# Performance work log

Hardware: AMD Instinct MI355X
Metric: run time of the kernel (lower is better)

## Reference

```python
import jax, jax.numpy as jnp
from jax import lax
import numpy as np

K_IN, K_OUT, K_STATE = 64, 64, 256
T_PRE, T_FWD, BATCH = 64, 80, 4096


def setup_inputs() -> dict:
    key = jax.random.key(0)
    ks = jax.random.split(key, 13)
    s = 0.05  # param scale for numerical stability of the recurrences
    return {
        "pre_x": jax.random.normal(ks[0], (T_PRE, BATCH, K_IN), jnp.float32),
        "pre_y": jax.random.normal(ks[1], (T_PRE, BATCH, K_OUT), jnp.float32),
        "forward_x": jax.random.normal(ks[2], (T_FWD, BATCH, K_IN), jnp.float32),
        "A_w": jax.random.normal(ks[3], (K_STATE, K_STATE), jnp.float32) * s,
        "A_b": jax.random.normal(ks[4], (K_STATE,), jnp.float32) * s,
        "B_w": jax.random.normal(ks[5], (K_STATE, K_IN), jnp.float32) * s,
        "B_b": jax.random.normal(ks[6], (K_STATE,), jnp.float32) * s,
        "C_w": jax.random.normal(ks[7], (K_OUT, K_STATE), jnp.float32) * s,
        "C_b": jax.random.normal(ks[8], (K_OUT,), jnp.float32) * s,
        "W_ih": jax.random.normal(ks[9], (K_STATE, K_IN + K_OUT), jnp.float32) * s,
        "b_ih": jax.random.normal(ks[10], (K_STATE,), jnp.float32) * s,
        "W_hh": jax.random.normal(ks[11], (K_STATE, K_STATE), jnp.float32) * s,
        "b_hh": jax.random.normal(ks[12], (K_STATE,), jnp.float32) * s,
    }


def reference(pre_x, pre_y, forward_x, A_w, A_b, B_w, B_b, C_w, C_b,
              W_ih, b_ih, W_hh, b_hh):
    # --- encoder: single-layer tanh RNN over concat(pre_x, pre_y), h0 = 0 ---
    xy = jnp.concatenate([pre_x, pre_y], axis=2)          # [T_pre, B, k_in+k_out]
    # precompute input projection for all steps (one big GEMM)
    inp_proj = xy @ W_ih.T + b_ih                          # [T_pre, B, k_state]

    def rnn_step(h, u):
        h = jnp.tanh(u + h @ W_hh.T + b_hh)
        return h, None

    h0 = jnp.zeros((pre_x.shape[1], W_hh.shape[0]), pre_x.dtype)
    hn, _ = lax.scan(rnn_step, h0, inp_proj)               # hn: [B, k_state]

    # --- state-space rollout: h_t = A h_{t-1} + B x_t ; y_t = C h_t ---
    Bx = forward_x @ B_w.T + (A_b + B_b)                   # fold both biases once

    def ss_step(h, bx):
        h = h @ A_w.T + bx
        return h, h

    _, hs = lax.scan(ss_step, hn, Bx)                      # [T_fwd, B, k_state]
    return hs @ C_w.T + C_b                                # [T_fwd, B, k_out]
```

## Files before the change

kernel.cpp:

```cpp
#include <hip/hip_runtime.h>

typedef __attribute__((ext_vector_type(8))) short short8;
typedef __attribute__((ext_vector_type(4))) float f32x4;

#define T_PRE 64
#define T_FWD 80
#define BATCHN 4096
#define PITCH 392

#define U_WRNN 0
#define U_WSS  98304
#define U_C    180224
#define U_END  196608
#define PREP_N 197120

__device__ __forceinline__ unsigned short bf1(float a) {
  unsigned ua = __float_as_uint(a);
  return (unsigned short)((ua + 0x7fffu + ((ua >> 16) & 1u)) >> 16);
}
__device__ __forceinline__ unsigned bfpack(float a, float b) {
  unsigned ua = __float_as_uint(a), ub = __float_as_uint(b);
  ua = (ua + 0x7fffu + ((ua >> 16) & 1u)) >> 16;
  ub = (ub + 0x7fffu + ((ub >> 16) & 1u)) >> 16;
  return ua | (ub << 16);
}
__device__ __forceinline__ float tanh_fast(float x) {
  float e = __expf(2.0f * x);
  return 1.0f - 2.0f * __builtin_amdgcn_rcpf(e + 1.0f);
}

__global__ void prep_kernel(const float* __restrict__ A_w, const float* __restrict__ A_b,
                            const float* __restrict__ B_w, const float* __restrict__ B_b,
                            const float* __restrict__ C_w,
                            const float* __restrict__ W_ih, const float* __restrict__ b_ih,
                            const float* __restrict__ W_hh, const float* __restrict__ b_hh,
                            unsigned short* __restrict__ ws) {
  int i = blockIdx.x * 256 + threadIdx.x;
  if (i < U_WSS) {
    int j = i / 384, k = i - j * 384;
    float v = (k < 256) ? W_hh[j * 256 + k] : W_ih[j * 128 + (k - 256)];
    ws[i] = bf1(v);
  } else if (i < U_C) {
    int ii = i - U_WSS;
    int j = ii / 320, k = ii - j * 320;
    float v = (k < 256) ? A_w[j * 256 + k] : B_w[j * 64 + (k - 256)];
    ws[i] = bf1(v);
  } else if (i < U_END) {
    int ii = i - U_C;
    int o = ii >> 8, k = ii & 255;
    ws[i] = bf1(C_w[o * 256 + k]);
  } else if (i < PREP_N) {
    float* fb = (float*)(ws + U_END);
    int j = i - U_END;
    fb[j] = (j < 256) ? (b_ih[j] + b_hh[j]) : (A_b[j - 256] + B_b[j - 256]);
  }
}

__global__ __launch_bounds__(256, 1) void rnn_ss_kernel(
    const float* __restrict__ pre_x, const float* __restrict__ pre_y,
    const float* __restrict__ fwd_x, const float* __restrict__ C_b,
    const unsigned short* __restrict__ ws, float* __restrict__ out) {
  __shared__ unsigned short xh[16 * PITCH];

  const int tid = threadIdx.x;
  const int lane = tid & 63;
  const int w = tid >> 6;
  const int col = lane & 15;
  const int q = lane >> 4;
  const int r0 = blockIdx.x * 16;
  const int srow = tid >> 4;
  const int sc4 = tid & 15;

  {
    unsigned* p = (unsigned*)xh;
#pragma unroll
    for (int it = 0; it < 8; ++it) {
      int i = tid + it * 256;
      int r = i >> 7, c = i & 127;
      p[r * (PITCH / 2) + c] = 0u;
    }
  }

  const float* fbias = (const float*)(ws + U_END);

  {
    short8 wf[4][12];
#pragma unroll
    for (int mt = 0; mt < 4; ++mt)
#pragma unroll
      for (int kf = 0; kf < 12; ++kf)
        wf[mt][kf] = *(const short8*)(ws + U_WRNN +
                       (size_t)(w * 64 + mt * 16 + col) * 384 + kf * 32 + q * 8);
    f32x4 br[4];
#pragma unroll
    for (int mt = 0; mt < 4; ++mt)
      br[mt] = *(const f32x4*)(fbias + w * 64 + mt * 16 + q * 4);

    {
      f32x4 px = *(const f32x4*)(pre_x + (size_t)(r0 + srow) * 64 + sc4 * 4);
      f32x4 py = *(const f32x4*)(pre_y + (size_t)(r0 + srow) * 64 + sc4 * 4);
      *(uint2*)&xh[srow * PITCH + 256 + sc4 * 4] = make_uint2(bfpack(px[0], px[1]), bfpack(px[2], px[3]));
      *(uint2*)&xh[srow * PITCH + 320 + sc4 * 4] = make_uint2(bfpack(py[0], py[1]), bfpack(py[2], py[3]));
    }

    for (int t = 0; t < T_PRE; ++t) {
      f32x4 npx, npy;
      if (t < T_PRE - 1) {
        npx = *(const f32x4*)(pre_x + ((size_t)(t + 1) * BATCHN + r0 + srow) * 64 + sc4 * 4);
        npy = *(const f32x4*)(pre_y + ((size_t)(t + 1) * BATCHN + r0 + srow) * 64 + sc4 * 4);
      }
      __syncthreads();
      short8 bfr[12];
#pragma unroll
      for (int kf = 0; kf < 12; ++kf)
        bfr[kf] = *(const short8*)&xh[col * PITCH + kf * 32 + q * 8];
      f32x4 acc[4];
#pragma unroll
      for (int mt = 0; mt < 4; ++mt) acc[mt] = br[mt];
#pragma unroll
      for (int kf = 0; kf < 12; ++kf)
#pragma unroll
        for (int mt = 0; mt < 4; ++mt)
          acc[mt] = __builtin_amdgcn_mfma_f32_16x16x32_bf16(wf[mt][kf], bfr[kf], acc[mt], 0, 0, 0);
      __syncthreads();
#pragma unroll
      for (int mt = 0; mt < 4; ++mt) {
        float t0 = tanh_fast(acc[mt][0]), t1 = tanh_fast(acc[mt][1]);
        float t2 = tanh_fast(acc[mt][2]), t3 = tanh_fast(acc[mt][3]);
        *(uint2*)&xh[col * PITCH + w * 64 + mt * 16 + q * 4] =
            make_uint2(bfpack(t0, t1), bfpack(t2, t3));
      }
      if (t < T_PRE - 1) {
        *(uint2*)&xh[srow * PITCH + 256 + sc4 * 4] = make_uint2(bfpack(npx[0], npx[1]), bfpack(npx[2], npx[3]));
        *(uint2*)&xh[srow * PITCH + 320 + sc4 * 4] = make_uint2(bfpack(npy[0], npy[1]), bfpack(npy[2], npy[3]));
      }
    }
  }

  {
    short8 sf[4][10];
#pragma unroll
    for (int mt = 0; mt < 4; ++mt)
#pragma unroll
      for (int kf = 0; kf < 10; ++kf)
        sf[mt][kf] = *(const short8*)(ws + U_WSS +
                       (size_t)(w * 64 + mt * 16 + col) * 320 + kf * 32 + q * 8);
    short8 cf[8];
#pragma unroll
    for (int kf = 0; kf < 8; ++kf)
      cf[kf] = *(const short8*)(ws + U_C + (size_t)(w * 16 + col) * 256 + kf * 32 + q * 8);
    f32x4 bs[4];
#pragma unroll
    for (int mt = 0; mt < 4; ++mt)
      bs[mt] = *(const f32x4*)(fbias + 256 + w * 64 + mt * 16 + q * 4);
    f32x4 cb = *(const f32x4*)(C_b + w * 16 + q * 4);

    {
      f32x4 fx = *(const f32x4*)(fwd_x + (size_t)(r0 + srow) * 64 + sc4 * 4);
      *(uint2*)&xh[srow * PITCH + 256 + sc4 * 4] = make_uint2(bfpack(fx[0], fx[1]), bfpack(fx[2], fx[3]));
    }

    for (int i = 0; i < T_FWD; ++i) {
      f32x4 nfx;
      if (i < T_FWD - 1)
        nfx = *(const f32x4*)(fwd_x + ((size_t)(i + 1) * BATCHN + r0 + srow) * 64 + sc4 * 4);
      __syncthreads();
      short8 bfr[10];
#pragma unroll
      for (int kf = 0; kf < 10; ++kf)
        bfr[kf] = *(const short8*)&xh[col * PITCH + kf * 32 + q * 8];
      f32x4 acc[4];
#pragma unroll
      for (int mt = 0; mt < 4; ++mt) acc[mt] = bs[mt];
#pragma unroll
      for (int kf = 0; kf < 10; ++kf)
#pragma unroll
        for (int mt = 0; mt < 4; ++mt)
          acc[mt] = __builtin_amdgcn_mfma_f32_16x16x32_bf16(sf[mt][kf], bfr[kf], acc[mt], 0, 0, 0);
      if (i >= 1) {
        f32x4 y = cb;
#pragma unroll
        for (int kf = 0; kf < 8; ++kf)
          y = __builtin_amdgcn_mfma_f32_16x16x32_bf16(cf[kf], bfr[kf], y, 0, 0, 0);
        *(f32x4*)(out + ((size_t)(i - 1) * BATCHN + r0 + col) * 64 + w * 16 + q * 4) = y;
      }
      __syncthreads();
#pragma unroll
      for (int mt = 0; mt < 4; ++mt)
        *(uint2*)&xh[col * PITCH + w * 64 + mt * 16 + q * 4] =
            make_uint2(bfpack(acc[mt][0], acc[mt][1]), bfpack(acc[mt][2], acc[mt][3]));
      if (i < T_FWD - 1)
        *(uint2*)&xh[srow * PITCH + 256 + sc4 * 4] = make_uint2(bfpack(nfx[0], nfx[1]), bfpack(nfx[2], nfx[3]));
    }

    __syncthreads();
    {
      short8 bfr[8];
#pragma unroll
      for (int kf = 0; kf < 8; ++kf)
        bfr[kf] = *(const short8*)&xh[col * PITCH + kf * 32 + q * 8];
      f32x4 y = cb;
#pragma unroll
      for (int kf = 0; kf < 8; ++kf)
        y = __builtin_amdgcn_mfma_f32_16x16x32_bf16(cf[kf], bfr[kf], y, 0, 0, 0);
      *(f32x4*)(out + ((size_t)(T_FWD - 1) * BATCHN + r0 + col) * 64 + w * 16 + q * 4) = y;
    }
  }
}

extern "C" void kernel_launch(void* const* d_in, const int* in_sizes, int n_in,
                              void* d_out, int out_size, void* d_ws, size_t ws_size,
                              hipStream_t stream) {
  const float* pre_x = (const float*)d_in[0];
  const float* pre_y = (const float*)d_in[1];
  const float* fwd_x = (const float*)d_in[2];
  const float* A_w   = (const float*)d_in[3];
  const float* A_b   = (const float*)d_in[4];
  const float* B_w   = (const float*)d_in[5];
  const float* B_b   = (const float*)d_in[6];
  const float* C_w   = (const float*)d_in[7];
  const float* C_b   = (const float*)d_in[8];
  const float* W_ih  = (const float*)d_in[9];
  const float* b_ih  = (const float*)d_in[10];
  const float* W_hh  = (const float*)d_in[11];
  const float* b_hh  = (const float*)d_in[12];
  unsigned short* ws = (unsigned short*)d_ws;
  float* out = (float*)d_out;

  prep_kernel<<<(PREP_N + 255) / 256, 256, 0, stream>>>(
      A_w, A_b, B_w, B_b, C_w, W_ih, b_ih, W_hh, b_hh, ws);
  rnn_ss_kernel<<<BATCHN / 16, 256, 0, stream>>>(pre_x, pre_y, fwd_x, C_b, ws, out);
}
```

Baseline: 316.4 us.

## Double-buffer recurrent state in LDS and split work across eight waves

Moves the block from 4 to 8 waves, so each wave owns 32 state rows (2 MFMA tiles) rather than 64. The hidden and input buffers are now ping-pong double-buffered, which removes one of the two barriers per timestep. X/Y staging is split across the two thread halves, and bf16 packing now uses the HIP intrinsic. The aim is a shorter serial critical path per step and better latency hiding. In exchange, the C-projection runs on only half the waves, and each step still pays a block-wide barrier across more waves.

```diff
diff --git a/kernel.cpp b/kernel.cpp
--- a/kernel.cpp
+++ b/kernel.cpp
@@ -1,4 +1,5 @@
 #include <hip/hip_runtime.h>
+#include <hip/hip_bf16.h>
 
 typedef __attribute__((ext_vector_type(8))) short short8;
 typedef __attribute__((ext_vector_type(4))) float f32x4;
@@ -6,7 +7,9 @@
 #define T_PRE 64
 #define T_FWD 80
 #define BATCHN 4096
-#define PITCH 392
+
+#define HP 264
+#define IP 136
 
 #define U_WRNN 0
 #define U_WSS  98304
@@ -18,11 +21,11 @@
   unsigned ua = __float_as_uint(a);
   return (unsigned short)((ua + 0x7fffu + ((ua >> 16) & 1u)) >> 16);
 }
-__device__ __forceinline__ unsigned bfpack(float a, float b) {
-  unsigned ua = __float_as_uint(a), ub = __float_as_uint(b);
-  ua = (ua + 0x7fffu + ((ua >> 16) & 1u)) >> 16;
-  ub = (ub + 0x7fffu + ((ub >> 16) & 1u)) >> 16;
-  return ua | (ub << 16);
+__device__ __forceinline__ unsigned pk(float a, float b) {
+  __hip_bfloat162 h = __float22bfloat162_rn(make_float2(a, b));
+  unsigned u;
+  __builtin_memcpy(&u, &h, 4);
+  return u;
 }
 __device__ __forceinline__ float tanh_fast(float x) {
   float e = __expf(2.0f * x);
@@ -56,11 +59,12 @@
   }
 }
 
-__global__ __launch_bounds__(256, 1) void rnn_ss_kernel(
+__global__ __launch_bounds__(512, 1) void rnn_ss_kernel(
     const float* __restrict__ pre_x, const float* __restrict__ pre_y,
     const float* __restrict__ fwd_x, const float* __restrict__ C_b,
     const unsigned short* __restrict__ ws, float* __restrict__ out) {
-  __shared__ unsigned short xh[16 * PITCH];
+  __shared__ unsigned short hbuf[2][16 * HP];
+  __shared__ unsigned short ibuf[2][16 * IP];
 
   const int tid = threadIdx.x;
   const int lane = tid & 63;
@@ -68,137 +72,152 @@
   const int col = lane & 15;
   const int q = lane >> 4;
   const int r0 = blockIdx.x * 16;
-  const int srow = tid >> 4;
+  const int srow = (tid & 255) >> 4;
   const int sc4 = tid & 15;
+  const bool xhalf = (tid >= 256);
+
+#pragma unroll
+  for (int it = 0; it < 2; ++it) {
+    int i = tid + it * 512;
+    int r = i >> 6, c = (i & 63) * 4;
+    *(uint2*)&hbuf[0][r * HP + c] = make_uint2(0u, 0u);
+  }
+
+  const float* fbias = (const float*)(ws + U_END);
+  int cur = 0;
 
   {
-    unsigned* p = (unsigned*)xh;
-#pragma unroll
-    for (int it = 0; it < 8; ++it) {
-      int i = tid + it * 256;
-      int r = i >> 7, c = i & 127;
-      p[r * (PITCH / 2) + c] = 0u;
-    }
-  }
-
-  const float* fbias = (const float*)(ws + U_END);
-
-  {
-    short8 wf[4][12];
-#pragma unroll
-    for (int mt = 0; mt < 4; ++mt)
+    short8 wf[2][12];
+#pragma unroll
+    for (int mt = 0; mt < 2; ++mt)
 #pragma unroll
       for (int kf = 0; kf < 12; ++kf)
         wf[mt][kf] = *(const short8*)(ws + U_WRNN +
-                       (size_t)(w * 64 + mt * 16 + col) * 384 + kf * 32 + q * 8);
-    f32x4 br[4];
-#pragma unroll
-    for (int mt = 0; mt < 4; ++mt)
-      br[mt] = *(const f32x4*)(fbias + w * 64 + mt * 16 + q * 4);
+                       (size_t)(w * 32 + mt * 16 + col) * 384 + kf * 32 + q * 8);
+    f32x4 br[2];
+#pragma unroll
+    for (int mt = 0; mt < 2; ++mt)
+      br[mt] = *(const f32x4*)(fbias + w * 32 + mt * 16 + q * 4);
 
     {
-      f32x4 px = *(const f32x4*)(pre_x + (size_t)(r0 + srow) * 64 + sc4 * 4);
-      f32x4 py = *(const f32x4*)(pre_y + (size_t)(r0 + srow) * 64 + sc4 * 4);
-      *(uint2*)&xh[srow * PITCH + 256 + sc4 * 4] = make_uint2(bfpack(px[0], px[1]), bfpack(px[2], px[3]));
-      *(uint2*)&xh[srow * PITCH + 320 + sc4 * 4] = make_uint2(bfpack(py[0], py[1]), bfpack(py[2], py[3]));
+      f32x4 v = xhalf ? *(const f32x4*)(pre_x + (size_t)(r0 + srow) * 64 + sc4 * 4)
+                      : *(const f32x4*)(pre_y + (size_t)(r0 + srow) * 64 + sc4 * 4);
+      *(uint2*)&ibuf[0][srow * IP + (xhalf ? 0 : 64) + sc4 * 4] =
+          make_uint2(pk(v[0], v[1]), pk(v[2], v[3]));
     }
 
     for (int t = 0; t < T_PRE; ++t) {
-      f32x4 npx, npy;
+      f32x4 nv;
+      bool do_stage = true;
       if (t < T_PRE - 1) {
-        npx = *(const f32x4*)(pre_x + ((size_t)(t + 1) * BATCHN + r0 + srow) * 64 + sc4 * 4);
-        npy = *(const f32x4*)(pre_y + ((size_t)(t + 1) * BATCHN + r0 + srow) * 64 + sc4 * 4);
+        nv = xhalf ? *(const f32x4*)(pre_x + ((size_t)(t + 1) * BATCHN + r0 + srow) * 64 + sc4 * 4)
+                   : *(const f32x4*)(pre_y + ((size_t)(t + 1) * BATCHN + r0 + srow) * 64 + sc4 * 4);
+      } else if (xhalf) {
+        nv = *(const f32x4*)(fwd_x + (size_t)(r0 + srow) * 64 + sc4 * 4);
+      } else {
+        do_stage = false;
       }
       __syncthreads();
+      const unsigned short* hc = hbuf[cur];
+      const unsigned short* ic = ibuf[cur];
       short8 bfr[12];
 #pragma unroll
+      for (int kf = 0; kf < 8; ++kf)
+        bfr[kf] = *(const short8*)&hc[col * HP + kf * 32 + q * 8];
+#pragma unroll
+      for (int kf = 8; kf < 12; ++kf)
+        bfr[kf] = *(const short8*)&ic[col * IP + (kf - 8) * 32 + q * 8];
+      f32x4 acc[2];
+#pragma unroll
+      for (int mt = 0; mt < 2; ++mt) acc[mt] = br[mt];
+#pragma unroll
       for (int kf = 0; kf < 12; ++kf)
-        bfr[kf] = *(const short8*)&xh[col * PITCH + kf * 32 + q * 8];
-      f32x4 acc[4];
-#pragma unroll
-      for (int mt = 0; mt < 4; ++mt) acc[mt] = br[mt];
-#pragma unroll
-      for (int kf = 0; kf < 12; ++kf)
-#pragma unroll
-        for (int mt = 0; mt < 4; ++mt)
+#pragma unroll
+        for (int mt = 0; mt < 2; ++mt)
           acc[mt] = __builtin_amdgcn_mfma_f32_16x16x32_bf16(wf[mt][kf], bfr[kf], acc[mt], 0, 0, 0);
-      __syncthreads();
-#pragma unroll
-      for (int mt = 0; mt < 4; ++mt) {
+      unsigned short* hn_ = hbuf[cur ^ 1];
+#pragma unroll
+      for (int mt = 0; mt < 2; ++mt) {
         float t0 = tanh_fast(acc[mt][0]), t1 = tanh_fast(acc[mt][1]);
         float t2 = tanh_fast(acc[mt][2]), t3 = tanh_fast(acc[mt][3]);
-        *(uint2*)&xh[col * PITCH + w * 64 + mt * 16 + q * 4] =
-            make_uint2(bfpack(t0, t1), bfpack(t2, t3));
+        *(uint2*)&hn_[col * HP + w * 32 + mt * 16 + q * 4] =
+            make_uint2(pk(t0, t1), pk(t2, t3));
       }
-      if (t < T_PRE - 1) {
-        *(uint2*)&xh[srow * PITCH + 256 + sc4 * 4] = make_uint2(bfpack(npx[0], npx[1]), bfpack(npx[2], npx[3]));
-        *(uint2*)&xh[srow * PITCH + 320 + sc4 * 4] = make_uint2(bfpack(npy[0], npy[1]), bfpack(npy[2], npy[3]));
-      }
+      if (do_stage)
+        *(uint2*)&ibuf[cur ^ 1][srow * IP + (xhalf ? 0 : 64) + sc4 * 4] =
+            make_uint2(pk(nv[0], nv[1]), pk(nv[2], nv[3]));
+      cur ^= 1;
     }
   }
 
   {
-    short8 sf[4][10];
-#pragma unroll
-    for (int mt = 0; mt < 4; ++mt)
+    short8 sf[2][10];
+#pragma unroll
+    for (int mt = 0; mt < 2; ++mt)
 #pragma unroll
       for (int kf = 0; kf < 10; ++kf)
         sf[mt][kf] = *(const short8*)(ws + U_WSS +
-                       (size_t)(w * 64 + mt * 16 + col) * 320 + kf * 32 + q * 8);
+                       (size_t)(w * 32 + mt * 16 + col) * 320 + kf * 32 + q * 8);
+    f32x4 bs[2];
+#pragma unroll
+    for (int mt = 0; mt < 2; ++mt)
+      bs[mt] = *(const f32x4*)(fbias + 256 + w * 32 + mt * 16 + q * 4);
     short8 cf[8];
-#pragma unroll
-    for (int kf = 0; kf < 8; ++kf)
-      cf[kf] = *(const short8*)(ws + U_C + (size_t)(w * 16 + col) * 256 + kf * 32 + q * 8);
-    f32x4 bs[4];
-#pragma unroll
-    for (int mt = 0; mt < 4; ++mt)
-      bs[mt] = *(const f32x4*)(fbias + 256 + w * 64 + mt * 16 + q * 4);
-    f32x4 cb = *(const f32x4*)(C_b + w * 16 + q * 4);
-
-    {
-      f32x4 fx = *(const f32x4*)(fwd_x + (size_t)(r0 + srow) * 64 + sc4 * 4);
-      *(uint2*)&xh[srow * PITCH + 256 + sc4 * 4] = make_uint2(bfpack(fx[0], fx[1]), bfpack(fx[2], fx[3]));
+    f32x4 cb;
+    if (w < 4) {
+#pragma unroll
+      for (int kf = 0; kf < 8; ++kf)
+        cf[kf] = *(const short8*)(ws + U_C + (size_t)(w * 16 + col) * 256 + kf * 32 + q * 8);
+      cb = *(const f32x4*)(C_b + w * 16 + q * 4);
     }
 
     for (int i = 0; i < T_FWD; ++i) {
-      f32x4 nfx;
-      if (i < T_FWD - 1)
-        nfx = *(const f32x4*)(fwd_x + ((size_t)(i + 1) * BATCHN + r0 + srow) * 64 + sc4 * 4);
+      f32x4 nv;
+      if (i < T_FWD - 1 && xhalf)
+        nv = *(const f32x4*)(fwd_x + ((size_t)(i + 1) * BATCHN + r0 + srow) * 64 + sc4 * 4);
       __syncthreads();
+      const unsigned short* hc = hbuf[cur];
+      const unsigned short* ic = ibuf[cur];
       short8 bfr[10];
 #pragma unroll
+      for (int kf = 0; kf < 8; ++kf)
+        bfr[kf] = *(const short8*)&hc[col * HP + kf * 32 + q * 8];
+#pragma unroll
+      for (int kf = 8; kf < 10; ++kf)
+        bfr[kf] = *(const short8*)&ic[col * IP + (kf - 8) * 32 + q * 8];
+      f32x4 acc[2];
+#pragma unroll
+      for (int mt = 0; mt < 2; ++mt) acc[mt] = bs[mt];
+#pragma unroll
       for (int kf = 0; kf < 10; ++kf)
-        bfr[kf] = *(const short8*)&xh[col * PITCH + kf * 32 + q * 8];
-      f32x4 acc[4];
-#pragma unroll
-      for (int mt = 0; mt < 4; ++mt) acc[mt] = bs[mt];
-#pragma unroll
-      for (int kf = 0; kf < 10; ++kf)
-#pragma unroll
-        for (int mt = 0; mt < 4; ++mt)
+#pragma unroll
+        for (int mt = 0; mt < 2; ++mt)
           acc[mt] = __builtin_amdgcn_mfma_f32_16x16x32_bf16(sf[mt][kf], bfr[kf], acc[mt], 0, 0, 0);
-      if (i >= 1) {
+      if (w < 4 && i >= 1) {
         f32x4 y = cb;
 #pragma unroll
         for (int kf = 0; kf < 8; ++kf)
           y = __builtin_amdgcn_mfma_f32_16x16x32_bf16(cf[kf], bfr[kf], y, 0, 0, 0);
         *(f32x4*)(out + ((size_t)(i - 1) * BATCHN + r0 + col) * 64 + w * 16 + q * 4) = y;
       }
-      __syncthreads();
-#pragma unroll
-      for (int mt = 0; mt < 4; ++mt)
-        *(uint2*)&xh[col * PITCH + w * 64 + mt * 16 + q * 4] =
-            make_uint2(bfpack(acc[mt][0], acc[mt][1]), bfpack(acc[mt][2], acc[mt][3]));
-      if (i < T_FWD - 1)
-        *(uint2*)&xh[srow * PITCH + 256 + sc4 * 4] = make_uint2(bfpack(nfx[0], nfx[1]), bfpack(nfx[2], nfx[3]));
+      unsigned short* hn_ = hbuf[cur ^ 1];
+#pragma unroll
+      for (int mt = 0; mt < 2; ++mt)
+        *(uint2*)&hn_[col * HP + w * 32 + mt * 16 + q * 4] =
+            make_uint2(pk(acc[mt][0], acc[mt][1]), pk(acc[mt][2], acc[mt][3]));
+      if (i < T_FWD - 1 && xhalf)
+        *(uint2*)&ibuf[cur ^ 1][srow * IP + sc4 * 4] =
+            make_uint2(pk(nv[0], nv[1]), pk(nv[2], nv[3]));
+      cur ^= 1;
     }
 
     __syncthreads();
-    {
+    if (w < 4) {
+      const unsigned short* hc = hbuf[cur];
       short8 bfr[8];
 #pragma unroll
       for (int kf = 0; kf < 8; ++kf)
-        bfr[kf] = *(const short8*)&xh[col * PITCH + kf * 32 + q * 8];
+        bfr[kf] = *(const short8*)&hc[col * HP + kf * 32 + q * 8];
       f32x4 y = cb;
 #pragma unroll
       for (int kf = 0; kf < 8; ++kf)
@@ -229,5 +248,5 @@
 
   prep_kernel<<<(PREP_N + 255) / 256, 256, 0, stream>>>(
       A_w, A_b, B_w, B_b, C_w, W_ih, b_ih, W_hh, b_hh, ws);
-  rnn_ss_kernel<<<BATCHN / 16, 256, 0, stream>>>(pre_x, pre_y, fwd_x, C_b, ws, out);
-}
+  rnn_ss_kernel<<<BATCHN / 16, 512, 0, stream>>>(pre_x, pre_y, fwd_x, C_b, ws, out);
+}
```

Measured after the change: 298.4 us. 5.7% less time.
